# Optimization experiments

Hardware: AMD Instinct MI355X
Metric: run time of the kernel (lower is better)

The kernel has to match this reference:

```python
import jax, jax.numpy as jnp
import numpy as np

DIM = 1536
NUM_HEADS = 16
HEAD_DIM = DIM // NUM_HEADS  # 96
ROPE_DIM = HEAD_DIM // 2     # 48
PT_SEQ = 32
FT_SEQ = 32
EPS = 1e-6


def _rope_tables():
    # VisionRotaryEmbedding(dim=48, pt_seq_len=32): 2D axial rotary tables
    f = 1.0 / (10000.0 ** (np.arange(0, ROPE_DIM, 2, dtype=np.float32)[: ROPE_DIM // 2] / ROPE_DIM))
    pos = np.arange(FT_SEQ, dtype=np.float32) / FT_SEQ * PT_SEQ
    freqs = pos[:, None] * f[None, :]                       # [32, 24]
    freqs = np.repeat(freqs, 2, axis=-1)                    # [32, 48] interleaved
    row = np.broadcast_to(freqs[:, None, :], (FT_SEQ, FT_SEQ, ROPE_DIM))
    col = np.broadcast_to(freqs[None, :, :], (FT_SEQ, FT_SEQ, ROPE_DIM))
    grid = np.concatenate([row, col], axis=-1).reshape(-1, HEAD_DIM)  # [1024, 96]
    return jnp.asarray(np.cos(grid)), jnp.asarray(np.sin(grid))


def _apply_rotary(x, cos, sin):
    # x: [B, S, H, D]; cos/sin: [S, D]; interleaved (use_real_unbind_dim=-1) rotation
    xr = x.reshape(*x.shape[:-1], -1, 2)
    x_rot = jnp.stack([-xr[..., 1], xr[..., 0]], axis=-1).reshape(x.shape)
    return x * cos[None, :, None, :] + x_rot * sin[None, :, None, :]


def _rms_norm(x, w):
    var = jnp.mean(jnp.square(x), axis=-1, keepdims=True)
    return x * jax.lax.rsqrt(var + EPS) * w


def setup_inputs() -> dict:
    key = jax.random.key(0)
    ks = jax.random.split(key, 12)
    s = 1.0 / np.sqrt(DIM)
    return {
        "hidden_states": jax.random.normal(ks[0], (8, 1024, DIM), dtype=jnp.float32),
        "Wq": jax.random.normal(ks[1], (DIM, DIM), dtype=jnp.float32) * s,
        "bq": jax.random.normal(ks[2], (DIM,), dtype=jnp.float32) * 0.01,
        "Wk": jax.random.normal(ks[3], (DIM, DIM), dtype=jnp.float32) * s,
        "bk": jax.random.normal(ks[4], (DIM,), dtype=jnp.float32) * 0.01,
        "Wv": jax.random.normal(ks[5], (DIM, DIM), dtype=jnp.float32) * s,
        "bv": jax.random.normal(ks[6], (DIM,), dtype=jnp.float32) * 0.01,
        "q_norm_w": jnp.ones((HEAD_DIM,), dtype=jnp.float32),
        "k_norm_w": jnp.ones((HEAD_DIM,), dtype=jnp.float32),
        "Wo": jax.random.normal(ks[7], (DIM, DIM), dtype=jnp.float32) * s,
        "bo": jax.random.normal(ks[8], (DIM,), dtype=jnp.float32) * 0.01,
    }


def reference(hidden_states, Wq, bq, Wk, bk, Wv, bv, q_norm_w, k_norm_w, Wo, bo):
    B, S, _ = hidden_states.shape
    cos, sin = _rope_tables()  # [S, HEAD_DIM], constants

    q = hidden_states @ Wq.T + bq
    k = hidden_states @ Wk.T + bk
    v = hidden_states @ Wv.T + bv
    q = q.reshape(B, S, NUM_HEADS, HEAD_DIM)
    k = k.reshape(B, S, NUM_HEADS, HEAD_DIM)
    v = v.reshape(B, S, NUM_HEADS, HEAD_DIM)

    q = _rms_norm(q, q_norm_w)
    k = _rms_norm(k, k_norm_w)
    q = _apply_rotary(q, cos, sin)
    k = _apply_rotary(k, cos, sin)

    scale = 1.0 / np.sqrt(HEAD_DIM)
    scores = jnp.einsum("bshd,bthd->bhst", q, k) * scale  # [B, H, S, S]
    probs = jax.nn.softmax(scores, axis=-1)
    out = jnp.einsum("bhst,bthd->bshd", probs, v)          # [B, S, H, D]
    out = out.reshape(B, S, DIM)
    return out @ Wo.T + bo
```

## Files before the change

### kernel.cpp

```cpp
#include <hip/hip_runtime.h>
#include <hip/hip_bf16.h>
#include <math.h>

typedef __hip_bfloat16 bf16;
typedef __attribute__((ext_vector_type(8))) short short8;
typedef __attribute__((ext_vector_type(4))) short short4v;
typedef __attribute__((ext_vector_type(4))) float f32x4;
typedef __attribute__((ext_vector_type(2))) int int2v;

#define MFMA16(a, b, c) __builtin_amdgcn_mfma_f32_16x16x32_bf16((a), (b), (c), 0, 0, 0)

typedef const __attribute__((address_space(1))) void GVOID;
typedef __attribute__((address_space(3))) void LVOID;

__device__ __forceinline__ float b2f(short s) {
    union { unsigned u; float f; } v;
    v.u = ((unsigned)(unsigned short)s) << 16;
    return v.f;
}
__device__ __forceinline__ short f2b(float f) {
    union { float f; unsigned u; } v;
    v.f = f;
    unsigned r = v.u + 0x7fffu + ((v.u >> 16) & 1u);
    return (short)(r >> 16);
}
__device__ __forceinline__ unsigned packbf2(float a, float b) {
    float2 t; t.x = a; t.y = b;
    __hip_bfloat162 h = __float22bfloat162_rn(t);
    union { __hip_bfloat162 h; unsigned u; } cv; cv.h = h;
    return cv.u;
}
__device__ __forceinline__ short bf2s(float x) {
    __hip_bfloat16 h = __float2bfloat16(x);
    union { __hip_bfloat16 h; short s; } cv; cv.h = h;
    return cv.s;
}

#if __has_builtin(__builtin_amdgcn_permlane32_swap)
__device__ __forceinline__ float addx32(float x) {
    union { float f; int i; } c; c.f = x;
    int2v r = __builtin_amdgcn_permlane32_swap(c.i, c.i, false, false);
    union { int i; float f; } a, b; a.i = r[0]; b.i = r[1];
    return a.f + b.f;
}
__device__ __forceinline__ float maxx32(float x) {
    union { float f; int i; } c; c.f = x;
    int2v r = __builtin_amdgcn_permlane32_swap(c.i, c.i, false, false);
    union { int i; float f; } a, b; a.i = r[0]; b.i = r[1];
    return fmaxf(a.f, b.f);
}
#else
__device__ __forceinline__ float addx32(float x) { return x + __shfl_xor(x, 32); }
__device__ __forceinline__ float maxx32(float x) { return fmaxf(x, __shfl_xor(x, 32)); }
#endif

__global__ __launch_bounds__(256) void prep_kernel(
    const unsigned* __restrict__ X,
    const void* __restrict__ bq, const void* __restrict__ bk,
    const void* __restrict__ bv, const void* __restrict__ bo,
    const void* __restrict__ qw, const void* __restrict__ kw,
    int* __restrict__ flag, float* __restrict__ biasqkv, float* __restrict__ boc,
    float* __restrict__ qwc, float* __restrict__ kwc,
    float* __restrict__ cosT, float* __restrict__ sinT)
{
    const int tid = threadIdx.x;
    if (blockIdx.x == 0) {
        __shared__ int cnt;
        if (tid == 0) cnt = 0;
        __syncthreads();
        unsigned w = X[tid];
        unsigned e = (w >> 7) & 0xFFu;
        if (e > 140u) atomicAdd(&cnt, 1);
        __syncthreads();
        const int f = (cnt >= 16) ? 1 : 0;
        if (tid == 0) *flag = f;
        for (int i = tid; i < 6336; i += 256) {
            const void* src; float* dst; int j;
            if (i < 4608) {
                int m = i / 1536; j = i - m * 1536;
                src = (m == 0) ? bq : (m == 1) ? bk : bv; dst = biasqkv + i;
            } else if (i < 6144) { j = i - 4608; src = bo; dst = boc + j; }
            else if (i < 6240)   { j = i - 6144; src = qw; dst = qwc + j; }
            else                 { j = i - 6240; src = kw; dst = kwc + j; }
            *dst = f ? ((const float*)src)[j] : b2f(((const short*)src)[j]);
        }
    } else {
        int idx = (blockIdx.x - 1) * 256 + tid;
        if (idx >= 1024 * 96) return;
        int p = idx / 96;
        int d = idx - p * 96;
        int r = p >> 5, c = p & 31;
        int inRow = (d < 48);
        int dd = inRow ? d : d - 48;
        float pos = inRow ? (float)r : (float)c;
        float ex = -(float)(dd & ~1) / 48.0f;
        float f = powf(10000.0f, ex);
        float ang = pos * f;
        cosT[idx] = cosf(ang);
        sinT[idx] = sinf(ang);
    }
}

__device__ __forceinline__ void canon8(const void* src, short* dst, int i, int f) {
    short8 o;
    if (f) {
        const float* s = (const float*)src + (size_t)i * 8;
#pragma unroll
        for (int j = 0; j < 8; ++j) o[j] = f2b(s[j]);
    } else {
        o = ((const short8*)src)[i];
    }
    ((short8*)dst)[i] = o;
}

__global__ __launch_bounds__(256) void canon_all_kernel(
    const void* __restrict__ X,
    const void* __restrict__ s0, const void* __restrict__ s1,
    const void* __restrict__ s2, const void* __restrict__ s3,
    short* __restrict__ dX,
    short* __restrict__ d0, short* __restrict__ d1,
    short* __restrict__ d2, short* __restrict__ d3,
    const int* __restrict__ flag)
{
    const int f = *flag;
    const int bid = blockIdx.x;
    if (bid < 6144) {
        canon8(X, dX, bid * 256 + threadIdx.x, f);
    } else {
        const int wb = bid - 6144;
        const int m = wb / 1152;
        const int i = (wb - m * 1152) * 256 + threadIdx.x;
        const void* src = (m == 0) ? s0 : (m == 1) ? s1 : (m == 2) ? s2 : s3;
        short* dst = (m == 0) ? d0 : (m == 1) ? d1 : (m == 2) ? d2 : d3;
        canon8(src, dst, i, f);
    }
}

__global__ __launch_bounds__(256) void gemm128_kernel(
    const bf16* __restrict__ A, const bf16* __restrict__ Bw,
    const float* __restrict__ bias,
    bf16* __restrict__ O0, bf16* __restrict__ O1, bf16* __restrict__ O2,
    int K, const int* __restrict__ outFlag)
{
    __shared__ __align__(16) short As[2][128 * 64];
    __shared__ __align__(16) short Bs[2][128 * 64];

    const int tid = threadIdx.x;
    const int lane = tid & 63, w = tid >> 6;
    const int wr = w >> 1, wc = w & 1;
    const int li = lane & 15, lg = lane >> 4;

    const int pp = blockIdx.y * gridDim.x + blockIdx.x;
    const int xcd = pp & 7;
    const int idx = pp >> 3;
    const int mb = xcd * 8 + (idx & 7);
    const int nb = idx >> 3;
    const long mBase = (long)mb * 128;
    const long nGlob = (long)nb * 128;

    const bf16* aSrc[4]; const bf16* bSrc[4]; int ldsOff[4];
#pragma unroll
    for (int u = 0; u < 4; ++u) {
        const int L = u * 4096 + tid * 16;
        const int S = L ^ (((L >> 7) & 7) << 4);
        const int srow = S >> 7;
        const int scol = (S & 127) >> 1;
        aSrc[u] = A + (mBase + srow) * K + scol;
        bSrc[u] = Bw + (nGlob + srow) * K + scol;
        ldsOff[u] = L >> 1;
    }
    const int rxor = (li & 7) << 4;
    int kidx[2];
#pragma unroll
    for (int ks = 0; ks < 2; ++ks)
        kidx[ks] = ((ks * 64 + lg * 16) ^ rxor) >> 1;

    f32x4 acc[4][4] = {};
    const int NT = K >> 6;

    auto stage = [&](int tt, int bb) {
        const long kc = (long)tt * 64;
#pragma unroll
        for (int u = 0; u < 4; ++u)
            __builtin_amdgcn_global_load_lds((GVOID*)(aSrc[u] + kc),
                                             (LVOID*)&As[bb][ldsOff[u]], 16, 0, 0);
#pragma unroll
        for (int u = 0; u < 4; ++u)
            __builtin_amdgcn_global_load_lds((GVOID*)(bSrc[u] + kc),
                                             (LVOID*)&Bs[bb][ldsOff[u]], 16, 0, 0);
    };

    stage(0, 0);
    asm volatile("s_waitcnt vmcnt(0)" ::: "memory");
    __builtin_amdgcn_s_barrier();
    asm volatile("" ::: "memory");

    for (int t = 0; t < NT; ++t) {
        const int cb = t & 1;
        if (t + 1 < NT) stage(t + 1, cb ^ 1);
        const short* Ab = &As[cb][0];
        const short* Bb = &Bs[cb][0];
#pragma unroll
        for (int ks = 0; ks < 2; ++ks) {
            short8 fa[4], fb[4];
#pragma unroll
            for (int m = 0; m < 4; ++m)
                fa[m] = *(const short8*)(Ab + (wr * 64 + m * 16 + li) * 64 + kidx[ks]);
#pragma unroll
            for (int n = 0; n < 4; ++n)
                fb[n] = *(const short8*)(Bb + (wc * 64 + n * 16 + li) * 64 + kidx[ks]);
            __builtin_amdgcn_sched_barrier(0);
            __builtin_amdgcn_s_setprio(1);
#pragma unroll
            for (int m = 0; m < 4; ++m)
#pragma unroll
                for (int n = 0; n < 4; ++n)
                    acc[m][n] = MFMA16(fa[m], fb[n], acc[m][n]);
            __builtin_amdgcn_s_setprio(0);
            __builtin_amdgcn_sched_barrier(0);
        }
        asm volatile("s_waitcnt vmcnt(0)" ::: "memory");
        __builtin_amdgcn_s_barrier();
        asm volatile("" ::: "memory");
    }

    const int f32out = outFlag ? *outFlag : 0;
    const int mat = nb / 12;
    const long colBase = nGlob - (long)mat * 1536;
    bf16* Ob = (mat == 0) ? O0 : (mat == 1) ? O1 : O2;
    if (f32out) {
        float* Cf = (float*)Ob;
#pragma unroll
        for (int n = 0; n < 4; ++n) {
            const long col = colBase + wc * 64 + n * 16 + li;
            const float bv = bias[nGlob + wc * 64 + n * 16 + li];
#pragma unroll
            for (int m = 0; m < 4; ++m) {
                const long row = mBase + wr * 64 + m * 16 + lg * 4;
#pragma unroll
                for (int i = 0; i < 4; ++i)
                    Cf[(row + i) * 1536 + col] = acc[m][n][i] + bv;
            }
        }
    } else {
#pragma unroll
        for (int n = 0; n < 4; ++n) {
            const long col = colBase + wc * 64 + n * 16 + li;
            const float bv = bias[nGlob + wc * 64 + n * 16 + li];
#pragma unroll
            for (int m = 0; m < 4; ++m) {
                const long row = mBase + wr * 64 + m * 16 + lg * 4;
#pragma unroll
                for (int i = 0; i < 4; ++i)
                    Ob[(row + i) * 1536 + col] = __float2bfloat16(acc[m][n][i] + bv);
            }
        }
    }
}

__global__ __launch_bounds__(256) void norm_rope2_kernel(
    bf16* __restrict__ Qb, bf16* __restrict__ Kb,
    const float* __restrict__ qwc, const float* __restrict__ kwc,
    const float* __restrict__ cosT, const float* __restrict__ sinT,
    float qscale)
{
    bf16* T = blockIdx.y ? Kb : Qb;
    const float* wgt = blockIdx.y ? kwc : qwc;
    const float scale = blockIdx.y ? 1.0f : qscale;

    const int row = blockIdx.x * 256 + threadIdx.x;
    const int tok = row >> 4;
    const int h = row & 15;
    const int spos = tok & 1023;
    bf16* p = T + (size_t)tok * 1536 + h * 96;

    float x[96];
#pragma unroll
    for (int v = 0; v < 12; ++v) {
        short8 t = *(const short8*)(p + v * 8);
#pragma unroll
        for (int j = 0; j < 8; ++j) x[v * 8 + j] = b2f(t[j]);
    }
    float ss = 0.f;
#pragma unroll
    for (int d = 0; d < 96; ++d) ss += x[d] * x[d];
    const float rn = scale / sqrtf(ss * (1.0f / 96.0f) + 1e-6f);

    const float* cr = cosT + spos * 96;
    const float* sr = sinT + spos * 96;

#pragma unroll
    for (int v = 0; v < 12; ++v) {
        short8 o;
#pragma unroll
        for (int j = 0; j < 8; j += 2) {
            const int d = v * 8 + j;
            const float x0 = x[d] * rn * wgt[d];
            const float x1 = x[d + 1] * rn * wgt[d + 1];
            o[j]     = f2b(x0 * cr[d] - x1 * sr[d]);
            o[j + 1] = f2b(x1 * cr[d + 1] + x0 * sr[d + 1]);
        }
        *(short8*)(p + v * 8) = o;
    }
}

__global__ __launch_bounds__(512, 2) void attn_kernel(
    const bf16* __restrict__ Q, const bf16* __restrict__ K,
    const bf16* __restrict__ V, bf16* __restrict__ O)
{
    __shared__ __align__(16) short Ks[2][64 * 96];
    __shared__ __align__(16) short Vt[2][96 * 64];
    __shared__ __align__(16) short Pl[8][16 * 64];

    const int tid = threadIdx.x;
    const int l = tid & 63, w = tid >> 6;
    const int li = l & 15, lg = l >> 4;

    const int p = blockIdx.x;
    const int lb = (p & 7) * 128 + (p >> 3);
    const int qt = lb & 7;
    const int bh = lb >> 3;
    const int b = bh >> 4, h = bh & 15;
    const size_t tokBase = (size_t)b * 1024;

    short8 aq[3];
    {
        const bf16* qp = Q + (tokBase + qt * 128 + w * 16 + li) * 1536 + h * 96;
#pragma unroll
        for (int kk = 0; kk < 3; ++kk)
            aq[kk] = *(const short8*)(qp + kk * 32 + lg * 8);
    }

    float m_r = -1e30f, l_r = 0.f;
    f32x4 o[6] = {};

    const bool kst = (w >= 4);
    int kr[3], km[3], kso[3];
#pragma unroll
    for (int u = 0; u < 3; ++u) {
        const int c = (tid - 256) + 256 * u;
        const int crr = c / 12;
        kr[u] = crr;
        km[u] = (c - crr * 12) * 8;
        kso[u] = (crr * 96 + km[u]) ^ ((crr & 7) << 3);
    }
    const int t2 = tid >> 3;
    const int dh = tid & 7;
    const bf16* vbase = V + (tokBase + 2 * t2) * 1536 + h * 96 + dh * 12;
    short* Plw = &Pl[w][0];

    const int kswz = (li & 7) << 3;
    const int vswz = ((li >> 1) & 7) << 3;

    short8 kreg[3];
    short4v vr0[3], vr1[3];
    auto loadT = [&](int tt) {
        if (kst) {
#pragma unroll
            for (int u = 0; u < 3; ++u)
                kreg[u] = *(const short8*)(K + (tokBase + tt + kr[u]) * 1536 + h * 96 + km[u]);
        } else {
            const bf16* vp = vbase + (size_t)tt * 1536;
#pragma unroll
            for (int u = 0; u < 3; ++u) {
                vr0[u] = *(const short4v*)(vp + u * 4);
                vr1[u] = *(const short4v*)(vp + 1536 + u * 4);
            }
        }
    };
    auto writeT = [&](int bb) {
        if (kst) {
#pragma unroll
            for (int u = 0; u < 3; ++u)
                *(short8*)&Ks[bb][kso[u]] = kreg[u];
        } else {
            unsigned* Vt32 = (unsigned*)&Vt[bb][0];
#pragma unroll
            for (int u = 0; u < 3; ++u)
#pragma unroll
                for (int j = 0; j < 4; ++j) {
                    const int d = dh * 12 + u * 4 + j;
                    const unsigned pk = ((unsigned)(unsigned short)vr0[u][j]) |
                                        (((unsigned)(unsigned short)vr1[u][j]) << 16);
                    Vt32[(d * 32 + t2) ^ (((d >> 1) & 7) << 2)] = pk;
                }
        }
    };

    loadT(0);
    writeT(0);
    loadT(64);
    __syncthreads();

    for (int t = 0; t < 16; ++t) {
        const int cb = t & 1;

        f32x4 s4[4] = {};
#pragma unroll
        for (int kk = 0; kk < 3; ++kk) {
#pragma unroll
            for (int kn = 0; kn < 4; ++kn) {
                short8 fk = *(const short8*)&Ks[cb][((kn * 16 + li) * 96 + kk * 32 + lg * 8) ^ kswz];
                s4[kn] = MFMA16(fk, aq[kk], s4[kn]);
            }
        }

        if (t < 15) writeT(cb ^ 1);
        if (t < 14) loadT((t + 2) * 64);

        {
            float mk[4];
#pragma unroll
            for (int kn = 0; kn < 4; ++kn)
                mk[kn] = fmaxf(fmaxf(s4[kn][0], s4[kn][1]),
                               fmaxf(s4[kn][2], s4[kn][3]));
            float pm = fmaxf(fmaxf(mk[0], mk[1]), fmaxf(mk[2], mk[3]));
            pm = fmaxf(pm, __shfl_xor(pm, 16));
            pm = maxx32(pm);

            float alpha = 1.0f;
            const bool need = (pm > m_r + 8.0f);
            if (need) { alpha = exp2f(m_r - pm); m_r = pm; }
            const float mn = m_r;

            float rs = 0.f;
            unsigned long long pq[4];
#pragma unroll
            for (int kn = 0; kn < 4; ++kn) {
                float p0 = exp2f(s4[kn][0] - mn);
                float p1 = exp2f(s4[kn][1] - mn);
                float p2 = exp2f(s4[kn][2] - mn);
                float p3 = exp2f(s4[kn][3] - mn);
                rs += (p0 + p1) + (p2 + p3);
                pq[kn] = ((unsigned long long)packbf2(p0, p1)) |
                         (((unsigned long long)packbf2(p2, p3)) << 32);
            }
            rs += __shfl_xor(rs, 16);
            rs = addx32(rs);
            l_r = l_r * alpha + rs;
            if (need) {
#pragma unroll
                for (int dn = 0; dn < 6; ++dn)
#pragma unroll
                    for (int i = 0; i < 4; ++i) o[dn][i] *= alpha;
            }
            const int rowS = li * 64;
#pragma unroll
            for (int kn = 0; kn < 4; ++kn)
                *(unsigned long long*)&Plw[(rowS + kn * 16 + lg * 4) ^ kswz] = pq[kn];
        }

#pragma unroll
        for (int kt = 0; kt < 2; ++kt) {
            short8 pa = *(const short8*)&Plw[(li * 64 + kt * 32 + lg * 8) ^ kswz];
#pragma unroll
            for (int dn = 0; dn < 6; ++dn) {
                short8 fv = *(const short8*)&Vt[cb][((dn * 16 + li) * 64 + kt * 32 + lg * 8) ^ vswz];
                o[dn] = MFMA16(fv, pa, o[dn]);
            }
        }

        __syncthreads();
    }

    {
        const float inv = 1.0f / l_r;
        const size_t row = tokBase + qt * 128 + w * 16 + li;
#pragma unroll
        for (int dn = 0; dn < 6; ++dn) {
            short4v ov;
#pragma unroll
            for (int i = 0; i < 4; ++i) ov[i] = bf2s(o[dn][i] * inv);
            *(short4v*)&O[row * 1536 + h * 96 + dn * 16 + lg * 4] = ov;
        }
    }
}

extern "C" void kernel_launch(void* const* d_in, const int* in_sizes, int n_in,
                              void* d_out, int out_size, void* d_ws, size_t ws_size,
                              hipStream_t stream) {
    const void* X  = d_in[0];
    const void* Wq = d_in[1];
    const void* bq = d_in[2];
    const void* Wk = d_in[3];
    const void* bk = d_in[4];
    const void* Wv = d_in[5];
    const void* bv = d_in[6];
    const void* qw = d_in[7];
    const void* kw = d_in[8];
    const void* Wo = d_in[9];
    const void* bo = d_in[10];

    char* ws = (char*)d_ws;
    size_t off = 0;
    int* flag = (int*)ws;                      off += 256;
    float* cosT = (float*)(ws + off);          off += 1024 * 96 * 4;
    float* sinT = (float*)(ws + off);          off += 1024 * 96 * 4;
    float* biasqkv = (float*)(ws + off);       off += 4608 * 4;
    float* boc  = (float*)(ws + off);          off += 1536 * 4;
    float* qwc  = (float*)(ws + off);          off += 128 * 4;
    float* kwc  = (float*)(ws + off);          off += 128 * 4;
    off = (off + 255) & ~(size_t)255;
    bf16* Wc  = (bf16*)(ws + off);             off += (size_t)4608 * 1536 * 2;
    bf16* Woc = (bf16*)(ws + off);             off += (size_t)1536 * 1536 * 2;
    bf16* Xc  = (bf16*)(ws + off);             off += (size_t)8192 * 1536 * 2;
    bf16* Qb  = (bf16*)(ws + off);             off += (size_t)8192 * 1536 * 2;
    bf16* Kb  = (bf16*)(ws + off);             off += (size_t)8192 * 1536 * 2;
    bf16* Vb  = (bf16*)(ws + off);             off += (size_t)8192 * 1536 * 2;
    bf16* AO  = Xc;

    prep_kernel<<<385, 256, 0, stream>>>((const unsigned*)X, bq, bk, bv, bo, qw, kw,
                                         flag, biasqkv, boc, qwc, kwc, cosT, sinT);

    canon_all_kernel<<<10752, 256, 0, stream>>>(
        X, Wq, Wk, Wv, Wo,
        (short*)Xc, (short*)Wc, (short*)(Wc + (size_t)1536 * 1536),
        (short*)(Wc + (size_t)2 * 1536 * 1536), (short*)Woc, flag);

    gemm128_kernel<<<dim3(36, 64), 256, 0, stream>>>(
        Xc, Wc, biasqkv, Qb, Kb, Vb, 1536, nullptr);

    const float qscale = (float)(0.10206207261596577 * 1.4426950408889634);
    norm_rope2_kernel<<<dim3(512, 2), 256, 0, stream>>>(Qb, Kb, qwc, kwc, cosT, sinT, qscale);

    attn_kernel<<<1024, 512, 0, stream>>>(Qb, Kb, Vb, AO);

    gemm128_kernel<<<dim3(12, 64), 256, 0, stream>>>(
        AO, Woc, boc, (bf16*)d_out, (bf16*)d_out, (bf16*)d_out, 1536, flag);
}
```

Baseline: 376.1 us.

## Keep softmax probabilities in registers by permuting K rows across MFMA tiles

Reorders which K rows each QK^T MFMA tile reads so that the score accumulator layout lines up with the B-operand layout the PV MFMA expects. The probabilities can then be packed straight from registers into the PV operand, with no round trip through a per-wave shared-memory buffer. This drops the P LDS array, its stores and loads, and the implied LDS traffic. The cost is extra index arithmetic and a different swizzle for the K fragment reads, which could change bank-conflict behaviour.

```diff
diff --git a/kernel.cpp b/kernel.cpp
--- a/kernel.cpp
+++ b/kernel.cpp
@@ -310,7 +310,6 @@
 {
     __shared__ __align__(16) short Ks[2][64 * 96];
     __shared__ __align__(16) short Vt[2][96 * 64];
-    __shared__ __align__(16) short Pl[8][16 * 64];
 
     const int tid = threadIdx.x;
     const int l = tid & 63, w = tid >> 6;
@@ -347,9 +346,20 @@
     const int t2 = tid >> 3;
     const int dh = tid & 7;
     const bf16* vbase = V + (tokBase + 2 * t2) * 1536 + h * 96 + dh * 12;
-    short* Plw = &Pl[w][0];
-
-    const int kswz = (li & 7) << 3;
+
+    const int rowbase = ((li >> 2) << 3) + (li & 3);
+    const int colb = lg * 8;
+    int frow[2][2];
+    int fswz[2];
+#pragma unroll
+    for (int kt = 0; kt < 2; ++kt)
+#pragma unroll
+        for (int hh = 0; hh < 2; ++hh)
+            frow[kt][hh] = (kt * 32 + 4 * hh + rowbase) * 96;
+#pragma unroll
+    for (int hh = 0; hh < 2; ++hh)
+        fswz[hh] = (4 * hh + (li & 3)) << 3;
+
     const int vswz = ((li >> 1) & 7) << 3;
 
     short8 kreg[3];
@@ -398,16 +408,20 @@
         f32x4 s4[4] = {};
 #pragma unroll
         for (int kk = 0; kk < 3; ++kk) {
-#pragma unroll
-            for (int kn = 0; kn < 4; ++kn) {
-                short8 fk = *(const short8*)&Ks[cb][((kn * 16 + li) * 96 + kk * 32 + lg * 8) ^ kswz];
-                s4[kn] = MFMA16(fk, aq[kk], s4[kn]);
-            }
+            const int ck = kk * 32 + colb;
+#pragma unroll
+            for (int kt = 0; kt < 2; ++kt)
+#pragma unroll
+                for (int hh = 0; hh < 2; ++hh) {
+                    short8 fk = *(const short8*)&Ks[cb][(frow[kt][hh] + ck) ^ fswz[hh]];
+                    s4[kt * 2 + hh] = MFMA16(fk, aq[kk], s4[kt * 2 + hh]);
+                }
         }
 
         if (t < 15) writeT(cb ^ 1);
         if (t < 14) loadT((t + 2) * 64);
 
+        unsigned pdw[4][2];
         {
             float mk[4];
 #pragma unroll
@@ -424,7 +438,6 @@
             const float mn = m_r;
 
             float rs = 0.f;
-            unsigned long long pq[4];
 #pragma unroll
             for (int kn = 0; kn < 4; ++kn) {
                 float p0 = exp2f(s4[kn][0] - mn);
@@ -432,8 +445,8 @@
                 float p2 = exp2f(s4[kn][2] - mn);
                 float p3 = exp2f(s4[kn][3] - mn);
                 rs += (p0 + p1) + (p2 + p3);
-                pq[kn] = ((unsigned long long)packbf2(p0, p1)) |
-                         (((unsigned long long)packbf2(p2, p3)) << 32);
+                pdw[kn][0] = packbf2(p0, p1);
+                pdw[kn][1] = packbf2(p2, p3);
             }
             rs += __shfl_xor(rs, 16);
             rs = addx32(rs);
@@ -444,19 +457,19 @@
 #pragma unroll
                     for (int i = 0; i < 4; ++i) o[dn][i] *= alpha;
             }
-            const int rowS = li * 64;
-#pragma unroll
-            for (int kn = 0; kn < 4; ++kn)
-                *(unsigned long long*)&Plw[(rowS + kn * 16 + lg * 4) ^ kswz] = pq[kn];
         }
 
 #pragma unroll
         for (int kt = 0; kt < 2; ++kt) {
-            short8 pa = *(const short8*)&Plw[(li * 64 + kt * 32 + lg * 8) ^ kswz];
+            union { unsigned u[4]; short8 s; } pa;
+            pa.u[0] = pdw[kt * 2][0];
+            pa.u[1] = pdw[kt * 2][1];
+            pa.u[2] = pdw[kt * 2 + 1][0];
+            pa.u[3] = pdw[kt * 2 + 1][1];
 #pragma unroll
             for (int dn = 0; dn < 6; ++dn) {
                 short8 fv = *(const short8*)&Vt[cb][((dn * 16 + li) * 64 + kt * 32 + lg * 8) ^ vswz];
-                o[dn] = MFMA16(fv, pa, o[dn]);
+                o[dn] = MFMA16(fv, pa.s, o[dn]);
             }
         }
 
```

New measurement: 376.7 us. About the same (+0.2%).
